# Optimization experiments

Measured on AMD Instinct MI355X. Metric: run time of the kernel, lower is better.

Reference implementation:

```python
import jax, jax.numpy as jnp
import numpy as np

B, D, H, DH, NQ, NK = 64, 768, 8, 128, 256, 256


def _ln(x, g, b, eps=1e-5):
    m = x.mean(-1, keepdims=True)
    v = ((x - m) ** 2).mean(-1, keepdims=True)
    return (x - m) / jnp.sqrt(v + eps) * g + b


def setup_inputs() -> dict:
    key = jax.random.key(0)
    ks = jax.random.split(key, 16)
    w = lambda k, s: jax.random.normal(k, s, jnp.float32) * 0.02
    return {
        'emb_cause': jax.random.normal(ks[0], (B, D), jnp.float32),
        'emb_action': jax.random.normal(ks[1], (B, D), jnp.float32),
        'tok_cause': jax.random.normal(ks[2], (B, NK, D), jnp.float32),
        'tok_effect': jax.random.normal(ks[3], (B, NQ, D), jnp.float32),
        'fuse_ln_g': jnp.ones(2 * D), 'fuse_ln_b': jnp.zeros(2 * D),
        'fuse_w1': w(ks[4], (2 * D, D)), 'fuse_b1': jnp.zeros(D),
        'fuse_w2': w(ks[5], (D, D)), 'fuse_b2': jnp.zeros(D),
        'delta_ln_g': jnp.ones(D), 'delta_ln_b': jnp.zeros(D),
        'delta_w': w(ks[6], (D, D)), 'delta_b': jnp.zeros(D),
        'qg_w': w(ks[7], (D, H * DH)), 'qg_b': jnp.zeros(H * DH),
        'kg_w': w(ks[8], (D, H * DH)), 'kg_b': jnp.zeros(H * DH),
        'eff_ln_g': jnp.ones(D), 'eff_ln_b': jnp.zeros(D),
        'eff_w1': w(ks[9], (D, D)), 'eff_b1': jnp.zeros(D),
        'eff_w2': w(ks[10], (D, D)), 'eff_b2': jnp.zeros(D),
        'u_w': w(ks[11], (D, H * DH)),
        'v_w': w(ks[12], (D, H * DH)),
        'logit_scale': jnp.zeros(()),
    }


def reference(emb_cause, emb_action, tok_cause, tok_effect,
              fuse_ln_g, fuse_ln_b, fuse_w1, fuse_b1, fuse_w2, fuse_b2,
              delta_ln_g, delta_ln_b, delta_w, delta_b,
              qg_w, qg_b, kg_w, kg_b,
              eff_ln_g, eff_ln_b, eff_w1, eff_b1, eff_w2, eff_b2,
              u_w, v_w, logit_scale):
    # fuse: LN -> Linear -> GELU(exact) -> Linear (dropout = identity, eval)
    ctx_in = jnp.concatenate([emb_cause, emb_action], axis=-1)  # (B, 2D)
    h = jax.nn.gelu(_ln(ctx_in, fuse_ln_g, fuse_ln_b) @ fuse_w1 + fuse_b1, approximate=False)
    ctx = h @ fuse_w2 + fuse_b2  # (B, D)

    delta_e = _ln(ctx, delta_ln_g, delta_ln_b) @ delta_w + delta_b  # (B, D)
    pooled_effect = tok_effect.mean(axis=1)  # (B, D)
    e_shifted = pooled_effect + delta_e

    eh = jax.nn.gelu(_ln(ctx, eff_ln_g, eff_ln_b) @ eff_w1 + eff_b1, approximate=False)
    effect_pred = eh @ eff_w2 + eff_b2  # (B, D)

    q_gate = 1.0 + jnp.tanh(jax.nn.silu(ctx @ qg_w + qg_b)).reshape(B, H, DH)
    k_gate = 1.0 + jnp.tanh(jax.nn.silu(ctx @ kg_w + kg_b)).reshape(B, H, DH)

    # logit bias: torch code materializes (B,H,Nq,Nk,Dh); equivalent math is a
    # per-head inner product u.v (independent of q) broadcast over Nq.
    u = (e_shifted @ u_w).reshape(B, H, DH)            # (B, H, Dh)
    v = (tok_cause @ v_w).reshape(B, NK, H, DH)        # (B, Nk, H, Dh)
    bias = jnp.einsum('bhd,bkhd->bhk', u, v) / np.float32(np.sqrt(DH))
    logit_bias = jnp.exp(logit_scale) * jnp.broadcast_to(bias[:, :, None, :], (B, H, NQ, NK))

    return (q_gate, k_gate, e_shifted, delta_e, logit_bias, effect_pred)
```

## Files before the change

### kernel.cpp

```cpp
#include <hip/hip_runtime.h>
#include <math.h>

#define TPB 256

typedef float vf4 __attribute__((ext_vector_type(4)));

__device__ __forceinline__ float gelu_f(float x) {
    return 0.5f * x * (1.0f + erff(x * 0.70710678118654752f));
}
__device__ __forceinline__ float gate_f(float x) {
    float si = x / (1.0f + expf(-x));
    return 1.0f + tanhf(si);
}

template <class XL>
__device__ __forceinline__ void gemm_tile(XL xload, const float* __restrict__ W, int Wld, int cb,
                                          int k0, int kslice, float* part, int totN, int gcol, int s,
                                          float* __restrict__ xs, float* __restrict__ wt)
{
    const int t = threadIdx.x;
    const int tr4 = (t >> 4) << 2;
    const int tc4 = (t & 15) << 2;
    float acc[4][4] = {{0.f,0.f,0.f,0.f},{0.f,0.f,0.f,0.f},{0.f,0.f,0.f,0.f},{0.f,0.f,0.f,0.f}};
    for (int kc = 0; kc < kslice; kc += 32) {
        for (int n = t; n < 2048; n += TPB) {
            int r = n >> 5, k = n & 31;
            xs[k * 68 + r] = xload(r, k0 + kc + k);
        }
        for (int n = t; n < 2048; n += TPB) {
            int k = n >> 6, c = n & 63;
            wt[k * 68 + c] = W[(size_t)(k0 + kc + k) * Wld + cb + c];
        }
        __syncthreads();
#pragma unroll
        for (int k = 0; k < 32; ++k) {
            float4 xv = *(const float4*)&xs[k * 68 + tr4];
            float4 wv = *(const float4*)&wt[k * 68 + tc4];
            acc[0][0] += xv.x * wv.x; acc[0][1] += xv.x * wv.y; acc[0][2] += xv.x * wv.z; acc[0][3] += xv.x * wv.w;
            acc[1][0] += xv.y * wv.x; acc[1][1] += xv.y * wv.y; acc[1][2] += xv.y * wv.z; acc[1][3] += xv.y * wv.w;
            acc[2][0] += xv.z * wv.x; acc[2][1] += xv.z * wv.y; acc[2][2] += xv.z * wv.z; acc[2][3] += xv.z * wv.w;
            acc[3][0] += xv.w * wv.x; acc[3][1] += xv.w * wv.y; acc[3][2] += xv.w * wv.z; acc[3][3] += xv.w * wv.w;
        }
        __syncthreads();
    }
    float* pp = part + (size_t)(s * 64 + tr4) * totN + gcol + tc4;
#pragma unroll
    for (int i = 0; i < 4; ++i)
#pragma unroll
        for (int j = 0; j < 4; ++j)
            pp[i * totN + j] = acc[i][j];
}

#define GEMM_LDS __shared__ float xs[32 * 68]; __shared__ float wt[32 * 68];

__global__ __launch_bounds__(256) void k_front(const float* __restrict__ ec, const float* __restrict__ ea,
                        const float* __restrict__ g, const float* __restrict__ bb,
                        float* __restrict__ o,
                        const float* __restrict__ tok_effect, float* __restrict__ pp)
{
    int t = threadIdx.x;
    if (blockIdx.x < 64) {
        int r = blockIdx.x;
        __shared__ float red[4];
        float v[6]; float sum = 0.f;
#pragma unroll
        for (int j = 0; j < 6; ++j) {
            int c = t + j * TPB;
            float x = (c < 768) ? ec[r * 768 + c] : ea[r * 768 + (c - 768)];
            v[j] = x; sum += x;
        }
#pragma unroll
        for (int o_ = 32; o_ > 0; o_ >>= 1) sum += __shfl_xor(sum, o_);
        if ((t & 63) == 0) red[t >> 6] = sum;
        __syncthreads();
        sum = red[0] + red[1] + red[2] + red[3];
        float mean = sum * (1.f / 1536.f);
        __syncthreads();
        float s2 = 0.f;
#pragma unroll
        for (int j = 0; j < 6; ++j) { float d = v[j] - mean; s2 += d * d; }
#pragma unroll
        for (int o_ = 32; o_ > 0; o_ >>= 1) s2 += __shfl_xor(s2, o_);
        if ((t & 63) == 0) red[t >> 6] = s2;
        __syncthreads();
        s2 = red[0] + red[1] + red[2] + red[3];
        float rstd = rsqrtf(s2 * (1.f / 1536.f) + 1e-5f);
#pragma unroll
        for (int j = 0; j < 6; ++j) {
            int c = t + j * TPB;
            o[r * 1536 + c] = (v[j] - mean) * rstd * g[c] + bb[c];
        }
    } else {
        int m = blockIdx.x - 64;
        int cch = m % 3, b = (m / 3) % 64, qz = m / 192;
        int c = cch * TPB + t;
        const float* base = tok_effect + (size_t)(b * 256 + qz * 64) * 768 + c;
        float s = 0.f;
#pragma unroll 16
        for (int q = 0; q < 64; ++q) s += base[(size_t)q * 768];
        pp[(qz * 64 + b) * 768 + c] = s;
    }
}

__global__ __launch_bounds__(256) void k_g1(const float* __restrict__ cat_ln, const float* __restrict__ w1,
                                            float* __restrict__ part1)
{
    GEMM_LDS;
    int ct = blockIdx.x % 12, s = blockIdx.x / 12;
    auto xl = [&](int r, int k) { return cat_ln[r * 1536 + k]; };
    gemm_tile(xl, w1, 768, ct * 64, s * 128, 128, part1, 768, ct * 64, s, xs, wt);
}

__global__ __launch_bounds__(256) void k_g2(const float* __restrict__ part1, const float* __restrict__ b1,
                                            const float* __restrict__ w2, float* __restrict__ part2)
{
    GEMM_LDS;
    int ct = blockIdx.x % 12, s = blockIdx.x / 12;
    auto xl = [&](int r, int k) {
        float v = b1[k];
#pragma unroll
        for (int q = 0; q < 12; ++q) v += part1[(size_t)(q * 64 + r) * 768 + k];
        return gelu_f(v);
    };
    gemm_tile(xl, w2, 768, ct * 64, s * 64, 64, part2, 768, ct * 64, s, xs, wt);
}

__global__ __launch_bounds__(256) void k_ln(const float* __restrict__ part2, const float* __restrict__ b2,
                        const float* __restrict__ dg, const float* __restrict__ db,
                        const float* __restrict__ eg, const float* __restrict__ eb,
                        float* __restrict__ ctx, float* __restrict__ od, float* __restrict__ oe)
{
    int r = blockIdx.x, t = threadIdx.x;
    __shared__ float red[4];
    float v[3]; float sum = 0.f;
#pragma unroll
    for (int j = 0; j < 3; ++j) {
        int c = t + j * TPB;
        float x = b2[c];
#pragma unroll
        for (int s = 0; s < 12; ++s) x += part2[(size_t)(s * 64 + r) * 768 + c];
        v[j] = x; sum += x;
        ctx[r * 768 + c] = x;
    }
#pragma unroll
    for (int o_ = 32; o_ > 0; o_ >>= 1) sum += __shfl_xor(sum, o_);
    if ((t & 63) == 0) red[t >> 6] = sum;
    __syncthreads();
    sum = red[0] + red[1] + red[2] + red[3];
    float mean = sum * (1.f / 768.f);
    __syncthreads();
    float s2 = 0.f;
#pragma unroll
    for (int j = 0; j < 3; ++j) { float d = v[j] - mean; s2 += d * d; }
#pragma unroll
    for (int o_ = 32; o_ > 0; o_ >>= 1) s2 += __shfl_xor(s2, o_);
    if ((t & 63) == 0) red[t >> 6] = s2;
    __syncthreads();
    s2 = red[0] + red[1] + red[2] + red[3];
    float rstd = rsqrtf(s2 * (1.f / 768.f) + 1e-5f);
#pragma unroll
    for (int j = 0; j < 3; ++j) {
        int c = t + j * TPB;
        float xh = (v[j] - mean) * rstd;
        od[r * 768 + c] = xh * dg[c] + db[c];
        oe[r * 768 + c] = xh * eg[c] + eb[c];
    }
}

struct GAArgs {
    const float *dln, *eln, *ctx, *delta_w, *eff_w1, *qg_w, *kg_w;
    float* partA;
};
__global__ __launch_bounds__(256) void k_gA(GAArgs A)
{
    GEMM_LDS;
    int ct = blockIdx.x % 56, s = blockIdx.x / 56;
    const float* X; const float* W; int Wld, cb;
    if (ct < 12)      { X = A.dln; W = A.delta_w; Wld = 768;  cb = ct * 64; }
    else if (ct < 24) { X = A.eln; W = A.eff_w1;  Wld = 768;  cb = (ct - 12) * 64; }
    else if (ct < 40) { X = A.ctx; W = A.qg_w;    Wld = 1024; cb = (ct - 24) * 64; }
    else              { X = A.ctx; W = A.kg_w;    Wld = 1024; cb = (ct - 40) * 64; }
    auto xl = [&](int r, int k) { return X[r * 768 + k]; };
    gemm_tile(xl, W, Wld, cb, s * 96, 96, A.partA, 3584, ct * 64, s, xs, wt);
}

struct MidArgs {
    const float *partA, *pp, *delta_b, *eff_b1, *qg_b, *kg_b, *eff_w2, *u_w;
    float *partB, *out_de, *out_es, *out_qg, *out_kg;
};
__global__ __launch_bounds__(256) void k_mid(MidArgs A)
{
    GEMM_LDS;
    const int t = threadIdx.x;
    if (blockIdx.x < 28) {
#pragma unroll
        for (int ii = 0; ii < 32; ++ii) {
            int idx = blockIdx.x * TPB + t + ii * 7168;
            int r = idx / 3584, c = idx - r * 3584;
            if (c >= 768 && c < 1536) continue;
            float v = 0.f;
#pragma unroll
            for (int q = 0; q < 8; ++q) v += A.partA[(size_t)(q * 64 + r) * 3584 + c];
            if (c < 768) {
                float de = v + A.delta_b[c];
                A.out_de[r * 768 + c] = de;
                float s4 = A.pp[r * 768 + c] + A.pp[(64 + r) * 768 + c]
                         + A.pp[(128 + r) * 768 + c] + A.pp[(192 + r) * 768 + c];
                A.out_es[r * 768 + c] = de + s4 * (1.f / 256.f);
            } else if (c < 2560) {
                A.out_qg[r * 1024 + (c - 1536)] = gate_f(v + A.qg_b[c - 1536]);
            } else {
                A.out_kg[r * 1024 + (c - 2560)] = gate_f(v + A.kg_b[c - 2560]);
            }
        }
    } else {
        int m = blockIdx.x - 28;
        int ct = m % 28, s = m / 28;
        if (ct < 12) {
            auto xl = [&](int r, int k) {
                float v = A.eff_b1[k];
#pragma unroll
                for (int q = 0; q < 8; ++q) v += A.partA[(size_t)(q * 64 + r) * 3584 + 768 + k];
                return gelu_f(v);
            };
            gemm_tile(xl, A.eff_w2, 768, ct * 64, s * 96, 96, A.partB, 1792, ct * 64, s, xs, wt);
        } else {
            auto xl = [&](int r, int k) {
                float v = A.delta_b[k];
#pragma unroll
                for (int q = 0; q < 8; ++q) v += A.partA[(size_t)(q * 64 + r) * 3584 + k];
                float s4 = A.pp[r * 768 + k] + A.pp[(64 + r) * 768 + k]
                         + A.pp[(128 + r) * 768 + k] + A.pp[(192 + r) * 768 + k];
                return v + s4 * (1.f / 256.f);
            };
            gemm_tile(xl, A.u_w, 1024, (ct - 12) * 64, s * 96, 96, A.partB, 1792, ct * 64, s, xs, wt);
        }
    }
}

__global__ __launch_bounds__(256) void k_tail(const float* __restrict__ partB, const float* __restrict__ eff_b2,
                                              const float* __restrict__ v_w,
                                              float* __restrict__ out_ep, float* __restrict__ wu)
{
    const int t = threadIdx.x;
    if (blockIdx.x < 6) {
#pragma unroll
        for (int ii = 0; ii < 32; ++ii) {
            int idx = blockIdx.x * TPB + t + ii * 1536;
            int r = idx / 768, c = idx - r * 768;
            float v = eff_b2[c];
#pragma unroll
            for (int q = 0; q < 8; ++q) v += partB[(size_t)(q * 64 + r) * 1792 + c];
            out_ep[r * 768 + c] = v;
        }
    } else {
        __shared__ float us[64 * 132];
        int m = blockIdx.x - 6;
        int h = m / 12, ctile = m % 12;
        for (int n = t; n < 8192; n += TPB) {
            int b = n >> 7, d = n & 127;
            float v = 0.f;
#pragma unroll
            for (int q = 0; q < 8; ++q) v += partB[(size_t)(q * 64 + b) * 1792 + 768 + h * 128 + d];
            us[b * 132 + d] = v;
        }
        __syncthreads();
        int c = ctile * 64 + (t >> 2);
        int bo = t & 3;
        const float* vr = v_w + (size_t)c * 1024 + h * 128;
        float acc[16];
#pragma unroll
        for (int i = 0; i < 16; ++i) acc[i] = 0.f;
        for (int d = 0; d < 128; d += 4) {
            float4 w4 = *(const float4*)(vr + d);
#pragma unroll
            for (int i = 0; i < 16; ++i) {
                const float* ub = &us[(4 * i + bo) * 132 + d];
                acc[i] += w4.x * ub[0] + w4.y * ub[1] + w4.z * ub[2] + w4.w * ub[3];
            }
        }
#pragma unroll
        for (int i = 0; i < 16; ++i) {
            int b = 4 * i + bo;
            wu[(b * 8 + h) * 768 + c] = acc[i];
        }
    }
}

__global__ __launch_bounds__(256) void k_biasbc(const float* __restrict__ tok_cause, const float* __restrict__ wu,
                         const float* __restrict__ ls_ptr, float* __restrict__ out_lb)
{
    int b = blockIdx.x, kt = blockIdx.y;
    __shared__ float wuh[8 * 768];
    __shared__ float bsm[8 * 32];
    for (int n = threadIdx.x; n < 6144; n += TPB)
        wuh[n] = wu[b * 6144 + n];
    __syncthreads();
    const int lane = threadIdx.x & 63, w = threadIdx.x >> 6;
    float4 wur[3][8];
#pragma unroll
    for (int j = 0; j < 3; ++j)
#pragma unroll
        for (int h = 0; h < 8; ++h)
            wur[j][h] = *(const float4*)&wuh[h * 768 + (lane + 64 * j) * 4];
    float scale = expf(ls_ptr[0]) * 0.08838834764831845f;
#pragma unroll
    for (int rr = 0; rr < 8; ++rr) {
        int rl = w * 8 + rr;
        int row = kt * 32 + rl;
        const float4* tr = (const float4*)(tok_cause + ((size_t)b * 256 + row) * 768);
        float4 t0 = tr[lane], t1 = tr[lane + 64], t2 = tr[lane + 128];
        float acc[8];
#pragma unroll
        for (int h = 0; h < 8; ++h) {
            acc[h] = t0.x * wur[0][h].x + t0.y * wur[0][h].y + t0.z * wur[0][h].z + t0.w * wur[0][h].w
                   + t1.x * wur[1][h].x + t1.y * wur[1][h].y + t1.z * wur[1][h].z + t1.w * wur[1][h].w
                   + t2.x * wur[2][h].x + t2.y * wur[2][h].y + t2.z * wur[2][h].z + t2.w * wur[2][h].w;
        }
#pragma unroll
        for (int h = 0; h < 8; ++h) {
            float vv = acc[h];
#pragma unroll
            for (int o_ = 32; o_ > 0; o_ >>= 1) vv += __shfl_xor(vv, o_);
            if (lane == 0) bsm[h * 32 + rl] = vv * scale;
        }
    }
    __syncthreads();
    const vf4* bs4 = (const vf4*)bsm;
    vf4* o4 = (vf4*)out_lb;
    int v = threadIdx.x & 7, sq0 = threadIdx.x >> 3;
#pragma unroll
    for (int it = 0; it < 64; ++it) {
        int seg = sq0 + it * 32;
        int h = seg >> 8, q = seg & 255;
        vf4 val = bs4[h * 8 + v];
        __builtin_nontemporal_store(val, &o4[(((size_t)(b * 8 + h) * 256 + q) << 6) + kt * 8 + v]);
    }
}

extern "C" void kernel_launch(void* const* d_in, const int* in_sizes, int n_in,
                              void* d_out, int out_size, void* d_ws, size_t ws_size,
                              hipStream_t stream)
{
    (void)in_sizes; (void)n_in; (void)out_size; (void)ws_size;
    const float* emb_cause  = (const float*)d_in[0];
    const float* emb_action = (const float*)d_in[1];
    const float* tok_cause  = (const float*)d_in[2];
    const float* tok_effect = (const float*)d_in[3];
    const float* fuse_ln_g  = (const float*)d_in[4];
    const float* fuse_ln_b  = (const float*)d_in[5];
    const float* fuse_w1    = (const float*)d_in[6];
    const float* fuse_b1    = (const float*)d_in[7];
    const float* fuse_w2    = (const float*)d_in[8];
    const float* fuse_b2    = (const float*)d_in[9];
    const float* delta_ln_g = (const float*)d_in[10];
    const float* delta_ln_b = (const float*)d_in[11];
    const float* delta_w    = (const float*)d_in[12];
    const float* delta_b    = (const float*)d_in[13];
    const float* qg_w       = (const float*)d_in[14];
    const float* qg_b       = (const float*)d_in[15];
    const float* kg_w       = (const float*)d_in[16];
    const float* kg_b       = (const float*)d_in[17];
    const float* eff_ln_g   = (const float*)d_in[18];
    const float* eff_ln_b   = (const float*)d_in[19];
    const float* eff_w1     = (const float*)d_in[20];
    const float* eff_b1     = (const float*)d_in[21];
    const float* eff_w2     = (const float*)d_in[22];
    const float* eff_b2     = (const float*)d_in[23];
    const float* u_w        = (const float*)d_in[24];
    const float* v_w        = (const float*)d_in[25];
    const float* logit_sc   = (const float*)d_in[26];

    float* ws = (float*)d_ws;
    float* cat_ln = ws + 0;
    float* ctx    = ws + 98304;
    float* dln    = ws + 147456;
    float* eln    = ws + 196608;
    float* pp     = ws + 245760;
    float* wu     = ws + 442368;

    float* out    = (float*)d_out;
    float* out_qg = out + 0;
    float* out_kg = out + 65536;
    float* out_es = out + 131072;
    float* out_de = out + 180224;
    float* out_lb = out + 229376;
    float* out_ep = out + 33783808;

    float* pbase = out_lb + 20000000;
    float* part1 = pbase;
    float* part2 = pbase + 589824;
    float* partA = pbase + 1179648;
    float* partB = pbase + 3014656;

    k_front<<<832, TPB, 0, stream>>>(emb_cause, emb_action, fuse_ln_g, fuse_ln_b, cat_ln,
                                     tok_effect, pp);
    k_g1<<<144, TPB, 0, stream>>>(cat_ln, fuse_w1, part1);
    k_g2<<<144, TPB, 0, stream>>>(part1, fuse_b1, fuse_w2, part2);
    k_ln<<<64, TPB, 0, stream>>>(part2, fuse_b2, delta_ln_g, delta_ln_b,
                                 eff_ln_g, eff_ln_b, ctx, dln, eln);
    {
        GAArgs A; A.dln = dln; A.eln = eln; A.ctx = ctx;
        A.delta_w = delta_w; A.eff_w1 = eff_w1; A.qg_w = qg_w; A.kg_w = kg_w; A.partA = partA;
        k_gA<<<448, TPB, 0, stream>>>(A);
    }
    {
        MidArgs M; M.partA = partA; M.pp = pp;
        M.delta_b = delta_b; M.eff_b1 = eff_b1; M.qg_b = qg_b; M.kg_b = kg_b;
        M.eff_w2 = eff_w2; M.u_w = u_w; M.partB = partB;
        M.out_de = out_de; M.out_es = out_es; M.out_qg = out_qg; M.out_kg = out_kg;
        k_mid<<<252, TPB, 0, stream>>>(M);
    }
    k_tail<<<102, TPB, 0, stream>>>(partB, eff_b2, v_w, out_ep, wu);
    k_biasbc<<<dim3(64, 8), TPB, 0, stream>>>(tok_cause, wu, logit_sc, out_lb);
}
```

Measured before the change: 172.7 us.

## Prefetch GEMM tiles into registers and fold LayerNorm apply into GEMM loaders

The shared GEMM tile routine now loads the next 32-wide K chunk of X and W into registers while the current chunk is being multiplied from LDS, overlapping global latency with compute. The LayerNorm kernels now write only per-row mean and rstd, and the consuming GEMMs apply normalization, gamma and beta inside their X loaders. This removes the writes and reads of the normalized cat_ln, dln and eln buffers. In exchange, each GEMM load does extra arithmetic and gamma/beta lookups, and register pressure rises from the 16 prefetch registers.

```diff
diff --git a/kernel.cpp b/kernel.cpp
--- a/kernel.cpp
+++ b/kernel.cpp
@@ -21,25 +21,38 @@
     const int t = threadIdx.x;
     const int tr4 = (t >> 4) << 2;
     const int tc4 = (t & 15) << 2;
+    const int a  = t >> 5, kk = t & 31;
+    const int wk = t >> 6, wc = t & 63;
+    float xv[8], wv[8];
+#pragma unroll
+    for (int j = 0; j < 8; ++j) {
+        xv[j] = xload(a + 8 * j, k0 + kk);
+        wv[j] = W[(size_t)(k0 + wk + 4 * j) * Wld + cb + wc];
+    }
     float acc[4][4] = {{0.f,0.f,0.f,0.f},{0.f,0.f,0.f,0.f},{0.f,0.f,0.f,0.f},{0.f,0.f,0.f,0.f}};
     for (int kc = 0; kc < kslice; kc += 32) {
-        for (int n = t; n < 2048; n += TPB) {
-            int r = n >> 5, k = n & 31;
-            xs[k * 68 + r] = xload(r, k0 + kc + k);
-        }
-        for (int n = t; n < 2048; n += TPB) {
-            int k = n >> 6, c = n & 63;
-            wt[k * 68 + c] = W[(size_t)(k0 + kc + k) * Wld + cb + c];
-        }
-        __syncthreads();
+#pragma unroll
+        for (int j = 0; j < 8; ++j) {
+            xs[kk * 68 + a + 8 * j] = xv[j];
+            wt[(wk + 4 * j) * 68 + wc] = wv[j];
+        }
+        __syncthreads();
+        int kn = kc + 32;
+        if (kn < kslice) {
+#pragma unroll
+            for (int j = 0; j < 8; ++j) {
+                xv[j] = xload(a + 8 * j, k0 + kn + kk);
+                wv[j] = W[(size_t)(k0 + kn + wk + 4 * j) * Wld + cb + wc];
+            }
+        }
 #pragma unroll
         for (int k = 0; k < 32; ++k) {
-            float4 xv = *(const float4*)&xs[k * 68 + tr4];
-            float4 wv = *(const float4*)&wt[k * 68 + tc4];
-            acc[0][0] += xv.x * wv.x; acc[0][1] += xv.x * wv.y; acc[0][2] += xv.x * wv.z; acc[0][3] += xv.x * wv.w;
-            acc[1][0] += xv.y * wv.x; acc[1][1] += xv.y * wv.y; acc[1][2] += xv.y * wv.z; acc[1][3] += xv.y * wv.w;
-            acc[2][0] += xv.z * wv.x; acc[2][1] += xv.z * wv.y; acc[2][2] += xv.z * wv.z; acc[2][3] += xv.z * wv.w;
-            acc[3][0] += xv.w * wv.x; acc[3][1] += xv.w * wv.y; acc[3][2] += xv.w * wv.z; acc[3][3] += xv.w * wv.w;
+            float4 xq = *(const float4*)&xs[k * 68 + tr4];
+            float4 wq = *(const float4*)&wt[k * 68 + tc4];
+            acc[0][0] += xq.x * wq.x; acc[0][1] += xq.x * wq.y; acc[0][2] += xq.x * wq.z; acc[0][3] += xq.x * wq.w;
+            acc[1][0] += xq.y * wq.x; acc[1][1] += xq.y * wq.y; acc[1][2] += xq.y * wq.z; acc[1][3] += xq.y * wq.w;
+            acc[2][0] += xq.z * wq.x; acc[2][1] += xq.z * wq.y; acc[2][2] += xq.z * wq.z; acc[2][3] += xq.z * wq.w;
+            acc[3][0] += xq.w * wq.x; acc[3][1] += xq.w * wq.y; acc[3][2] += xq.w * wq.z; acc[3][3] += xq.w * wq.w;
         }
         __syncthreads();
     }
@@ -54,8 +67,7 @@
 #define GEMM_LDS __shared__ float xs[32 * 68]; __shared__ float wt[32 * 68];
 
 __global__ __launch_bounds__(256) void k_front(const float* __restrict__ ec, const float* __restrict__ ea,
-                        const float* __restrict__ g, const float* __restrict__ bb,
-                        float* __restrict__ o,
+                        float* __restrict__ stats1,
                         const float* __restrict__ tok_effect, float* __restrict__ pp)
 {
     int t = threadIdx.x;
@@ -84,11 +96,9 @@
         if ((t & 63) == 0) red[t >> 6] = s2;
         __syncthreads();
         s2 = red[0] + red[1] + red[2] + red[3];
-        float rstd = rsqrtf(s2 * (1.f / 1536.f) + 1e-5f);
-#pragma unroll
-        for (int j = 0; j < 6; ++j) {
-            int c = t + j * TPB;
-            o[r * 1536 + c] = (v[j] - mean) * rstd * g[c] + bb[c];
+        if (t == 0) {
+            stats1[2 * r]     = mean;
+            stats1[2 * r + 1] = rsqrtf(s2 * (1.f / 1536.f) + 1e-5f);
         }
     } else {
         int m = blockIdx.x - 64;
@@ -102,13 +112,20 @@
     }
 }
 
-__global__ __launch_bounds__(256) void k_g1(const float* __restrict__ cat_ln, const float* __restrict__ w1,
-                                            float* __restrict__ part1)
+struct G1Args {
+    const float *ec, *ea, *stats1, *flg, *flb, *w1;
+    float* part1;
+};
+__global__ __launch_bounds__(256) void k_g1(G1Args A)
 {
     GEMM_LDS;
     int ct = blockIdx.x % 12, s = blockIdx.x / 12;
-    auto xl = [&](int r, int k) { return cat_ln[r * 1536 + k]; };
-    gemm_tile(xl, w1, 768, ct * 64, s * 128, 128, part1, 768, ct * 64, s, xs, wt);
+    auto xl = [&](int r, int k) {
+        float raw = (k < 768) ? A.ec[r * 768 + k] : A.ea[r * 768 + (k - 768)];
+        float m = A.stats1[2 * r], rs = A.stats1[2 * r + 1];
+        return (raw - m) * rs * A.flg[k] + A.flb[k];
+    };
+    gemm_tile(xl, A.w1, 768, ct * 64, s * 128, 128, A.part1, 768, ct * 64, s, xs, wt);
 }
 
 __global__ __launch_bounds__(256) void k_g2(const float* __restrict__ part1, const float* __restrict__ b1,
@@ -126,9 +143,7 @@
 }
 
 __global__ __launch_bounds__(256) void k_ln(const float* __restrict__ part2, const float* __restrict__ b2,
-                        const float* __restrict__ dg, const float* __restrict__ db,
-                        const float* __restrict__ eg, const float* __restrict__ eb,
-                        float* __restrict__ ctx, float* __restrict__ od, float* __restrict__ oe)
+                                            float* __restrict__ ctx, float* __restrict__ stats2)
 {
     int r = blockIdx.x, t = threadIdx.x;
     __shared__ float red[4];
@@ -157,31 +172,39 @@
     if ((t & 63) == 0) red[t >> 6] = s2;
     __syncthreads();
     s2 = red[0] + red[1] + red[2] + red[3];
-    float rstd = rsqrtf(s2 * (1.f / 768.f) + 1e-5f);
-#pragma unroll
-    for (int j = 0; j < 3; ++j) {
-        int c = t + j * TPB;
-        float xh = (v[j] - mean) * rstd;
-        od[r * 768 + c] = xh * dg[c] + db[c];
-        oe[r * 768 + c] = xh * eg[c] + eb[c];
+    if (t == 0) {
+        stats2[2 * r]     = mean;
+        stats2[2 * r + 1] = rsqrtf(s2 * (1.f / 768.f) + 1e-5f);
     }
 }
 
 struct GAArgs {
-    const float *dln, *eln, *ctx, *delta_w, *eff_w1, *qg_w, *kg_w;
+    const float *ctx, *stats2, *dg, *db, *eg, *eb;
+    const float *delta_w, *eff_w1, *qg_w, *kg_w;
     float* partA;
 };
 __global__ __launch_bounds__(256) void k_gA(GAArgs A)
 {
     GEMM_LDS;
     int ct = blockIdx.x % 56, s = blockIdx.x / 56;
-    const float* X; const float* W; int Wld, cb;
-    if (ct < 12)      { X = A.dln; W = A.delta_w; Wld = 768;  cb = ct * 64; }
-    else if (ct < 24) { X = A.eln; W = A.eff_w1;  Wld = 768;  cb = (ct - 12) * 64; }
-    else if (ct < 40) { X = A.ctx; W = A.qg_w;    Wld = 1024; cb = (ct - 24) * 64; }
-    else              { X = A.ctx; W = A.kg_w;    Wld = 1024; cb = (ct - 40) * 64; }
-    auto xl = [&](int r, int k) { return X[r * 768 + k]; };
-    gemm_tile(xl, W, Wld, cb, s * 96, 96, A.partA, 3584, ct * 64, s, xs, wt);
+    if (ct < 12) {
+        auto xl = [&](int r, int k) {
+            float m = A.stats2[2 * r], rs = A.stats2[2 * r + 1];
+            return (A.ctx[r * 768 + k] - m) * rs * A.dg[k] + A.db[k];
+        };
+        gemm_tile(xl, A.delta_w, 768, ct * 64, s * 96, 96, A.partA, 3584, ct * 64, s, xs, wt);
+    } else if (ct < 24) {
+        auto xl = [&](int r, int k) {
+            float m = A.stats2[2 * r], rs = A.stats2[2 * r + 1];
+            return (A.ctx[r * 768 + k] - m) * rs * A.eg[k] + A.eb[k];
+        };
+        gemm_tile(xl, A.eff_w1, 768, (ct - 12) * 64, s * 96, 96, A.partA, 3584, ct * 64, s, xs, wt);
+    } else {
+        auto xl = [&](int r, int k) { return A.ctx[r * 768 + k]; };
+        const float* W = (ct < 40) ? A.qg_w : A.kg_w;
+        int cb = (ct < 40) ? (ct - 24) * 64 : (ct - 40) * 64;
+        gemm_tile(xl, W, 1024, cb, s * 96, 96, A.partA, 3584, ct * 64, s, xs, wt);
+    }
 }
 
 struct MidArgs {
@@ -372,12 +395,11 @@
     const float* logit_sc   = (const float*)d_in[26];
 
     float* ws = (float*)d_ws;
-    float* cat_ln = ws + 0;
-    float* ctx    = ws + 98304;
-    float* dln    = ws + 147456;
-    float* eln    = ws + 196608;
-    float* pp     = ws + 245760;
-    float* wu     = ws + 442368;
+    float* ctx    = ws + 0;
+    float* pp     = ws + 49152;
+    float* wu     = ws + 245760;
+    float* stats1 = ws + 638976;
+    float* stats2 = ws + 639104;
 
     float* out    = (float*)d_out;
     float* out_qg = out + 0;
@@ -393,14 +415,17 @@
     float* partA = pbase + 1179648;
     float* partB = pbase + 3014656;
 
-    k_front<<<832, TPB, 0, stream>>>(emb_cause, emb_action, fuse_ln_g, fuse_ln_b, cat_ln,
-                                     tok_effect, pp);
-    k_g1<<<144, TPB, 0, stream>>>(cat_ln, fuse_w1, part1);
+    k_front<<<832, TPB, 0, stream>>>(emb_cause, emb_action, stats1, tok_effect, pp);
+    {
+        G1Args A; A.ec = emb_cause; A.ea = emb_action; A.stats1 = stats1;
+        A.flg = fuse_ln_g; A.flb = fuse_ln_b; A.w1 = fuse_w1; A.part1 = part1;
+        k_g1<<<144, TPB, 0, stream>>>(A);
+    }
     k_g2<<<144, TPB, 0, stream>>>(part1, fuse_b1, fuse_w2, part2);
-    k_ln<<<64, TPB, 0, stream>>>(part2, fuse_b2, delta_ln_g, delta_ln_b,
-                                 eff_ln_g, eff_ln_b, ctx, dln, eln);
+    k_ln<<<64, TPB, 0, stream>>>(part2, fuse_b2, ctx, stats2);
     {
-        GAArgs A; A.dln = dln; A.eln = eln; A.ctx = ctx;
+        GAArgs A; A.ctx = ctx; A.stats2 = stats2;
+        A.dg = delta_ln_g; A.db = delta_ln_b; A.eg = eff_ln_g; A.eb = eff_ln_b;
         A.delta_w = delta_w; A.eff_w1 = eff_w1; A.qg_w = qg_w; A.kg_w = kg_w; A.partA = partA;
         k_gA<<<448, TPB, 0, stream>>>(A);
     }
```

After: 143.9 us. 1.2x faster.
